# Optimization experiments

Hardware: AMD Instinct MI355X
Metric: run time of the kernel (lower is better)

The kernel has to match this reference:

```python
import jax, jax.numpy as jnp
import numpy as np

T, B, V, S = 2000, 32, 1000, 200
NEG = -1e30  # log-zero stand-in (avoids inf-inf NaNs)


def setup_inputs() -> dict:
    key = jax.random.key(0)
    k1, k2, k3 = jax.random.split(key, 3)
    logits = jax.random.normal(k1, (T, B, V), dtype=jnp.float32)
    targets = jax.random.randint(k2, (B, S), 1, V, dtype=jnp.int32)  # non-blank labels (blank=0)
    input_lengths = jnp.full((B,), T, dtype=jnp.int32)
    target_lengths = jax.random.randint(k3, (B,), S // 2, S + 1, dtype=jnp.int32)
    return {"logits": logits, "targets": targets,
            "input_lengths": input_lengths, "target_lengths": target_lengths}


def _ctc_loss_mean(logits, targets, input_lengths, target_lengths):
    # CTC forward (log-semiring) over the blank-interleaved lattice; equals
    # k2 intersect_dense + get_tot_scores with unpruned beam, blank=0.
    Tn, Bn, Vn = logits.shape
    Sn = targets.shape[1]
    L = 2 * Sn + 1  # extended label sequence: blank, l1, blank, l2, ...
    log_probs = jax.nn.log_softmax(logits, axis=-1)  # [T,B,V]

    ext = jnp.zeros((Bn, L), targets.dtype).at[:, 1::2].set(targets)  # [B,L]
    pos = jnp.arange(L)
    # skip (s-2 -> s) allowed at odd s>=3 when the label differs from previous label
    diff = jnp.concatenate([jnp.ones((Bn, 2), bool), ext[:, 2:] != ext[:, :-2]], axis=1)
    allow_skip = (pos[None, :] % 2 == 1) & (pos[None, :] >= 3) & diff  # [B,L]

    lp0 = jnp.take_along_axis(log_probs[0], ext, axis=1)  # [B,L]
    a0 = jnp.full((Bn, L), NEG, log_probs.dtype)
    a0 = a0.at[:, 0].set(lp0[:, 0]).at[:, 1].set(lp0[:, 1])

    def step(alpha, xs):
        lp_t, t = xs  # lp_t: [B,V]
        lp = jnp.take_along_axis(lp_t, ext, axis=1)  # [B,L]
        s1 = jnp.concatenate([jnp.full((Bn, 1), NEG, alpha.dtype), alpha[:, :-1]], axis=1)
        s2 = jnp.where(allow_skip,
                       jnp.concatenate([jnp.full((Bn, 2), NEG, alpha.dtype), alpha[:, :-2]], axis=1),
                       NEG)
        new = jnp.logaddexp(jnp.logaddexp(alpha, s1), s2) + lp
        valid = (t < input_lengths)[:, None]
        return jnp.where(valid, new, alpha), None

    alpha, _ = jax.lax.scan(step, a0, (log_probs[1:], jnp.arange(1, Tn)))

    end = 2 * target_lengths  # final blank state; end-1 is final label state
    a_last = jnp.take_along_axis(alpha, end[:, None], axis=1)[:, 0]
    a_prev = jnp.take_along_axis(alpha, (end - 1)[:, None], axis=1)[:, 0]
    loss = -jnp.logaddexp(a_last, a_prev).astype(jnp.float32)  # [B]
    # reduction='mean' (k2 default): divide by target length, then batch mean
    return (loss / target_lengths.astype(jnp.float32)).mean()


def reference(logits, targets, input_lengths, target_lengths):
    return _ctc_loss_mean(logits, targets, input_lengths, target_lengths)
```

## Files before the change

kernel.cpp:

```cpp
#include <hip/hip_runtime.h>
#include <math.h>

#define TT 2000
#define BB 32
#define VV 1000
#define SS 200
#define LROW 256

#if defined(__has_builtin) && __has_builtin(__builtin_amdgcn_ldexpf)
__device__ __forceinline__ float ldx(float x, int e) { return __builtin_amdgcn_ldexpf(x, e); }
#else
__device__ __forceinline__ float ldx(float x, int e) { return ldexpf(x, e); }
#endif

__global__ __launch_bounds__(256) void ctc_phase1(
    const float* __restrict__ logits, const int* __restrict__ targets,
    float* __restrict__ PL, float* __restrict__ PB, float* __restrict__ out)
{
    if (blockIdx.x == 0 && threadIdx.x == 0) out[0] = 0.f;
    int wid  = (blockIdx.x * 256 + threadIdx.x) >> 6;
    int lane = threadIdx.x & 63;
    if (wid >= TT * BB) return;
    const float* __restrict__ row = logits + (size_t)wid * VV;
    int b = wid & (BB - 1);

    int i0 = 4 * lane;
    float4 v0 = *(const float4*)(row + i0);
    float4 v1 = *(const float4*)(row + i0 + 256);
    float4 v2 = *(const float4*)(row + i0 + 512);
    int i3 = i0 + 768;
    float4 v3 = *(const float4*)(row + (i3 < VV ? i3 : 0));
    if (i3 >= VV) { v3.x = v3.y = v3.z = v3.w = -1e30f; }

    float M = fmaxf(fmaxf(fmaxf(v0.x, v0.y), fmaxf(v0.z, v0.w)),
                    fmaxf(fmaxf(fmaxf(v1.x, v1.y), fmaxf(v1.z, v1.w)),
                          fmaxf(fmaxf(fmaxf(v2.x, v2.y), fmaxf(v2.z, v2.w)),
                                fmaxf(fmaxf(v3.x, v3.y), fmaxf(v3.z, v3.w)))));
    #pragma unroll
    for (int off = 1; off < 64; off <<= 1) M = fmaxf(M, __shfl_xor(M, off));

    float s = __expf(v0.x - M) + __expf(v0.y - M) + __expf(v0.z - M) + __expf(v0.w - M)
            + __expf(v1.x - M) + __expf(v1.y - M) + __expf(v1.z - M) + __expf(v1.w - M)
            + __expf(v2.x - M) + __expf(v2.y - M) + __expf(v2.z - M) + __expf(v2.w - M)
            + __expf(v3.x - M) + __expf(v3.y - M) + __expf(v3.z - M) + __expf(v3.w - M);
    #pragma unroll
    for (int off = 1; off < 64; off <<= 1) s += __shfl_xor(s, off);
    float inv = 1.0f / s;

    const int* __restrict__ tg = targets + b * SS;
    #pragma unroll
    for (int k = 0; k < 4; k++) {
        int j = k * 64 + lane;
        int lbl = (j < SS) ? tg[j] : 0;
        float g = row[lbl];
        float pv = (j < SS) ? (__expf(g - M) * inv) : 0.f;
        PL[(size_t)wid * LROW + j] = pv;
    }
    if (lane == 0) PB[wid] = __expf(row[0] - M) * inv;
}


#define STEP(q, qb) do {                                    \
    float sh_  = __shfl_up(a7, 1);                          \
    float prev = ldx(sh_, dB);             \
    float n0 = (a0 + prev) * (qb);                          \
    float n1 = fmaf(mk0, prev, a1 + a0) * (q).x;            \
    float n2 = (a2 + a1) * (qb);                            \
    float n3 = fmaf(mk1, a1, a3 + a2) * (q).y;              \
    float n4 = (a4 + a3) * (qb);                            \
    float n5 = fmaf(mk2, a3, a5 + a4) * (q).z;              \
    float n6 = (a6 + a5) * (qb);                            \
    float n7 = fmaf(mk3, a5, a7 + a6) * (q).w;              \
    a0=n0; a1=n1; a2=n2; a3=n3; a4=n4; a5=n5; a6=n6; a7=n7; } while (0)

#define RESCALE() do {                                      \
    float mx = fmaxf(fmaxf(fmaxf(a0,a1),fmaxf(a2,a3)),fmaxf(fmaxf(a4,a5),fmaxf(a6,a7))); \
    unsigned eb = (__float_as_uint(mx) >> 23) & 255u;       \
    int de = (eb == 0u) ? 0 : ((int)eb - 127);              \
    a0 = ldx(a0, -de); a1 = ldx(a1, -de); a2 = ldx(a2, -de); a3 = ldx(a3, -de); \
    a4 = ldx(a4, -de); a5 = ldx(a5, -de); a6 = ldx(a6, -de); a7 = ldx(a7, -de); \
    e_acc += de;                                            \
    int she = __shfl_up(e_acc, 1);                          \
    if (eb == 0u) e_acc = she;         \
    dB = (lane == 0) ? -100000 : (she - e_acc); } while (0)

#define LOADG(PLb, PBb, basestep) do {                      \
    _Pragma("unroll")                                       \
    for (int k_ = 0; k_ < 16; k_++) {                       \
        int t_ = (basestep) + k_ + 1;                       \
        t_ = (t_ < Tb) ? t_ : (Tb - 1);                     \
        const float4* rp_ = (const float4*)(PL + ((size_t)t_ * BB + b) * LROW); \
        PLb[k_] = rp_[lane];                                \
        PBb[k_] = PB[t_ * BB + b];                          \
    } } while (0)

__global__ __launch_bounds__(64, 1) void ctc_phase2(
    const float* __restrict__ PL, const float* __restrict__ PB,
    const int* __restrict__ targets, const int* __restrict__ ilen,
    const int* __restrict__ tlen, float* __restrict__ out)
{
    int b = blockIdx.x;
    int lane = threadIdx.x;
    const int* __restrict__ tg = targets + b * SS;

    float mk0 = 0.f, mk1 = 0.f, mk2 = 0.f, mk3 = 0.f;
    {
        int u0 = 4 * lane;
        if (u0 >= 1 && u0 < SS) mk0 = (tg[u0] != tg[u0 - 1]) ? 1.f : 0.f;
        if (u0 + 1 < SS)        mk1 = (tg[u0 + 1] != tg[u0]) ? 1.f : 0.f;
        if (u0 + 2 < SS)        mk2 = (tg[u0 + 2] != tg[u0 + 1]) ? 1.f : 0.f;
        if (u0 + 3 < SS)        mk3 = (tg[u0 + 3] != tg[u0 + 2]) ? 1.f : 0.f;
    }
    int Tb = ilen[b];
    int tl = tlen[b];

    float a0=0,a1=0,a2=0,a3=0,a4=0,a5=0,a6=0,a7=0;
    int e_acc = 0;
    int dB = (lane == 0) ? -100000 : 0;

    {
        const float4* r0 = (const float4*)(PL + (size_t)b * LROW);
        float4 p0 = r0[lane];
        float pb0 = PB[b];
        if (lane == 0) { a0 = pb0; a1 = p0.x; }
    }

    int nsteps = Tb - 1;
    float4 plA[16]; float pbA[16];
    float4 plB[16]; float pbB[16];

    LOADG(plA, pbA, 0);
    int s = 0;
    for (; s + 32 <= nsteps; s += 32) {
        LOADG(plB, pbB, s + 16);
        #pragma unroll
        for (int k = 0; k < 16; k++) { STEP(plA[k], pbA[k]); if ((k & 3) == 3) RESCALE(); }
        LOADG(plA, pbA, s + 32);
        #pragma unroll
        for (int k = 0; k < 16; k++) { STEP(plB[k], pbB[k]); if ((k & 3) == 3) RESCALE(); }
    }
    int rem = nsteps - s;
    int r1 = rem < 16 ? rem : 16;
    #pragma unroll
    for (int k = 0; k < 16; k++) { if (k < r1) { STEP(plA[k], pbA[k]); if ((k & 3) == 3) RESCALE(); } }
    if (rem > 16) {
        LOADG(plB, pbB, s + 16);
        int r2 = rem - 16;
        #pragma unroll
        for (int k = 0; k < 16; k++) { if (k < r2) { STEP(plB[k], pbB[k]); if ((k & 3) == 3) RESCALE(); } }
    }

    __shared__ float sa[64][8];
    __shared__ int   se[64];
    sa[lane][0]=a0; sa[lane][1]=a1; sa[lane][2]=a2; sa[lane][3]=a3;
    sa[lane][4]=a4; sa[lane][5]=a5; sa[lane][6]=a6; sa[lane][7]=a7;
    se[lane] = e_acc;
    __syncthreads();
    if (lane == 0) {
        int end = 2 * tl;
        float ae = sa[end >> 3][end & 7];
        float am = sa[(end - 1) >> 3][(end - 1) & 7];
        int   ee = se[end >> 3];
        int   em = se[(end - 1) >> 3];
        float val = ae + ldx(am, em - ee);
        double lb = -((double)logf(val) + (double)ee * 0.6931471805599453);
        float contrib = (float)(lb / ((double)tl * (double)BB));
        atomicAdd(out, contrib);
    }
}

extern "C" void kernel_launch(void* const* d_in, const int* in_sizes, int n_in,
                              void* d_out, int out_size, void* d_ws, size_t ws_size,
                              hipStream_t stream)
{
    const float* logits  = (const float*)d_in[0];
    const int*   targets = (const int*)d_in[1];
    const int*   ilen    = (const int*)d_in[2];
    const int*   tlen    = (const int*)d_in[3];
    float* out = (float*)d_out;

    float* PL = (float*)d_ws;
    float* PB = PL + (size_t)TT * BB * LROW;

    ctc_phase1<<<(TT * BB) / 4, 256, 0, stream>>>(logits, targets, PL, PB, out);
    ctc_phase2<<<BB, 64, 0, stream>>>(PL, PB, targets, ilen, tlen, out);
}
```

Baseline: 649.5 us.

## Use rolling per-step prefetch in CTC recursion and vectorize label gather

The serial phase-2 recursion replaces its two 16-deep batched load buffers with a rolling ring of 16 registers. Each step's slot is refilled with the load for 16 steps ahead immediately after use, so memory latency stays hidden continuously rather than in bursts. Phase 1 now reads targets as int4 and writes the per-lane probabilities as a single float4 store instead of four scalar loops. The ldexp builtin selection is also dropped in favour of plain ldexpf, which may compile to slower code in the rescale path.

```diff
diff --git a/kernel.cpp b/kernel.cpp
--- a/kernel.cpp
+++ b/kernel.cpp
@@ -7,11 +7,7 @@
 #define SS 200
 #define LROW 256
 
-#if defined(__has_builtin) && __has_builtin(__builtin_amdgcn_ldexpf)
-__device__ __forceinline__ float ldx(float x, int e) { return __builtin_amdgcn_ldexpf(x, e); }
-#else
 __device__ __forceinline__ float ldx(float x, int e) { return ldexpf(x, e); }
-#endif
 
 __global__ __launch_bounds__(256) void ctc_phase1(
     const float* __restrict__ logits, const int* __restrict__ targets,
@@ -48,14 +44,18 @@
     float inv = 1.0f / s;
 
     const int* __restrict__ tg = targets + b * SS;
-    #pragma unroll
-    for (int k = 0; k < 4; k++) {
-        int j = k * 64 + lane;
-        int lbl = (j < SS) ? tg[j] : 0;
-        float g = row[lbl];
-        float pv = (j < SS) ? (__expf(g - M) * inv) : 0.f;
-        PL[(size_t)wid * LROW + j] = pv;
-    }
+    int j0 = 4 * lane;
+    int4 tt = ((const int4*)tg)[(j0 < SS) ? lane : 0];
+    int l0 = (j0     < SS) ? tt.x : 0;
+    int l1 = (j0 + 1 < SS) ? tt.y : 0;
+    int l2 = (j0 + 2 < SS) ? tt.z : 0;
+    int l3 = (j0 + 3 < SS) ? tt.w : 0;
+    float4 w;
+    w.x = (j0     <= SS) ? (__expf(row[l0] - M) * inv) : 0.f;
+    w.y = (j0 + 1 <= SS) ? (__expf(row[l1] - M) * inv) : 0.f;
+    w.z = (j0 + 2 <= SS) ? (__expf(row[l2] - M) * inv) : 0.f;
+    w.w = (j0 + 3 <= SS) ? (__expf(row[l3] - M) * inv) : 0.f;
+    ((float4*)(PL + (size_t)wid * LROW))[lane] = w;
     if (lane == 0) PB[wid] = __expf(row[0] - M) * inv;
 }
 
@@ -84,15 +84,13 @@
     if (eb == 0u) e_acc = she;         \
     dB = (lane == 0) ? -100000 : (she - e_acc); } while (0)
 
-#define LOADG(PLb, PBb, basestep) do {                      \
-    _Pragma("unroll")                                       \
-    for (int k_ = 0; k_ < 16; k_++) {                       \
-        int t_ = (basestep) + k_ + 1;                       \
-        t_ = (t_ < Tb) ? t_ : (Tb - 1);                     \
-        const float4* rp_ = (const float4*)(PL + ((size_t)t_ * BB + b) * LROW); \
-        PLb[k_] = rp_[lane];                                \
-        PBb[k_] = PB[t_ * BB + b];                          \
-    } } while (0)
+#define PF(Q, Bv, tnext) do {                               \
+    int tn_ = (tnext); tn_ = (tn_ < Tb) ? tn_ : (Tb - 1);   \
+    Q  = ((const float4*)(PLb + (size_t)tn_ * (BB * LROW)))[lane]; \
+    Bv = PBb[(size_t)tn_ * BB]; } while (0)
+
+#define UNIT(Q, Bv, i) do { STEP(Q, Bv); if (((i) & 3) == 3) RESCALE(); PF(Q, Bv, t + 16 + (i)); } while (0)
+#define TAILU(Q, Bv, i) do { if ((i) < rem) { STEP(Q, Bv); if (((i) & 3) == 3) RESCALE(); } } while (0)
 
 __global__ __launch_bounds__(64, 1) void ctc_phase2(
     const float* __restrict__ PL, const float* __restrict__ PB,
@@ -118,37 +116,36 @@
     int e_acc = 0;
     int dB = (lane == 0) ? -100000 : 0;
 
+    const float* __restrict__ PLb = PL + (size_t)b * LROW;
+    const float* __restrict__ PBb = PB + b;
+
     {
-        const float4* r0 = (const float4*)(PL + (size_t)b * LROW);
-        float4 p0 = r0[lane];
-        float pb0 = PB[b];
+        float4 p0 = ((const float4*)PLb)[lane];
+        float pb0 = PBb[0];
         if (lane == 0) { a0 = pb0; a1 = p0.x; }
     }
 
     int nsteps = Tb - 1;
-    float4 plA[16]; float pbA[16];
-    float4 plB[16]; float pbB[16];
+    float4 q0,q1,q2,q3,q4,q5,q6,q7,q8,q9,q10,q11,q12,q13,q14,q15;
+    float  c0,c1,c2,c3,c4,c5,c6,c7,c8,c9,c10,c11,c12,c13,c14,c15;
 
-    LOADG(plA, pbA, 0);
-    int s = 0;
-    for (; s + 32 <= nsteps; s += 32) {
-        LOADG(plB, pbB, s + 16);
-        #pragma unroll
-        for (int k = 0; k < 16; k++) { STEP(plA[k], pbA[k]); if ((k & 3) == 3) RESCALE(); }
-        LOADG(plA, pbA, s + 32);
-        #pragma unroll
-        for (int k = 0; k < 16; k++) { STEP(plB[k], pbB[k]); if ((k & 3) == 3) RESCALE(); }
+    PF(q0,c0,1);   PF(q1,c1,2);   PF(q2,c2,3);   PF(q3,c3,4);
+    PF(q4,c4,5);   PF(q5,c5,6);   PF(q6,c6,7);   PF(q7,c7,8);
+    PF(q8,c8,9);   PF(q9,c9,10);  PF(q10,c10,11); PF(q11,c11,12);
+    PF(q12,c12,13); PF(q13,c13,14); PF(q14,c14,15); PF(q15,c15,16);
+
+    int t = 1;
+    for (; t + 15 <= nsteps; t += 16) {
+        UNIT(q0,c0,0);   UNIT(q1,c1,1);   UNIT(q2,c2,2);   UNIT(q3,c3,3);
+        UNIT(q4,c4,4);   UNIT(q5,c5,5);   UNIT(q6,c6,6);   UNIT(q7,c7,7);
+        UNIT(q8,c8,8);   UNIT(q9,c9,9);   UNIT(q10,c10,10); UNIT(q11,c11,11);
+        UNIT(q12,c12,12); UNIT(q13,c13,13); UNIT(q14,c14,14); UNIT(q15,c15,15);
     }
-    int rem = nsteps - s;
-    int r1 = rem < 16 ? rem : 16;
-    #pragma unroll
-    for (int k = 0; k < 16; k++) { if (k < r1) { STEP(plA[k], pbA[k]); if ((k & 3) == 3) RESCALE(); } }
-    if (rem > 16) {
-        LOADG(plB, pbB, s + 16);
-        int r2 = rem - 16;
-        #pragma unroll
-        for (int k = 0; k < 16; k++) { if (k < r2) { STEP(plB[k], pbB[k]); if ((k & 3) == 3) RESCALE(); } }
-    }
+    int rem = nsteps - t + 1;
+    TAILU(q0,c0,0);   TAILU(q1,c1,1);   TAILU(q2,c2,2);   TAILU(q3,c3,3);
+    TAILU(q4,c4,4);   TAILU(q5,c5,5);   TAILU(q6,c6,6);   TAILU(q7,c7,7);
+    TAILU(q8,c8,8);   TAILU(q9,c9,9);   TAILU(q10,c10,10); TAILU(q11,c11,11);
+    TAILU(q12,c12,12); TAILU(q13,c13,13); TAILU(q14,c14,14); TAILU(q15,c15,15);
 
     __shared__ float sa[64][8];
     __shared__ int   se[64];
```

After: 595.8 us. -8.3%, faster.
